# Kernel tuning notes

Measured on AMD Instinct MI355X. Metric: run time of the kernel, lower is better.

Reference implementation:

```python
import jax, jax.numpy as jnp
import numpy as np

CROP_H = 7
CROP_W = 7
EXTRAP = 0.0  # module hardcodes 0 when calling CropAndResizeFunction


def _crop_and_resize(image, boxes, box_ind):
    """TF-style crop_and_resize.
    image: (N,C,H,W) float; boxes: (M,4) normalized (y1,x1,y2,x2); box_ind: (M,) int32.
    Returns (M,C,CROP_H,CROP_W).
    """
    N, C, H, W = image.shape
    dt = image.dtype
    y1, x1, y2, x2 = boxes[:, 0], boxes[:, 1], boxes[:, 2], boxes[:, 3]
    ii = jnp.arange(CROP_H, dtype=dt)
    jj = jnp.arange(CROP_W, dtype=dt)
    # sample coordinates in feature-map space, shape (M, CROP_H) / (M, CROP_W)
    y = y1[:, None] * (H - 1) + ii[None, :] * ((y2 - y1) * (H - 1) / (CROP_H - 1))[:, None]
    x = x1[:, None] * (W - 1) + jj[None, :] * ((x2 - x1) * (W - 1) / (CROP_W - 1))[:, None]
    valid_y = (y >= 0) & (y <= H - 1)
    valid_x = (x >= 0) & (x <= W - 1)
    yt_f = jnp.floor(y)
    xt_f = jnp.floor(x)
    y_lerp = y - yt_f  # (M, oh)
    x_lerp = x - xt_f  # (M, ow)
    yt = jnp.clip(yt_f, 0, H - 1).astype(jnp.int32)
    yb = jnp.clip(jnp.ceil(y), 0, H - 1).astype(jnp.int32)
    xl = jnp.clip(xt_f, 0, W - 1).astype(jnp.int32)
    xr = jnp.clip(jnp.ceil(x), 0, W - 1).astype(jnp.int32)
    img = jnp.transpose(image, (0, 2, 3, 1))  # (N,H,W,C) for clean gather
    b = box_ind[:, None, None]                # (M,1,1)
    tl = img[b, yt[:, :, None], xl[:, None, :]]  # (M,oh,ow,C)
    tr = img[b, yt[:, :, None], xr[:, None, :]]
    bl = img[b, yb[:, :, None], xl[:, None, :]]
    br = img[b, yb[:, :, None], xr[:, None, :]]
    xl_w = x_lerp[:, None, :, None]
    top = tl + (tr - tl) * xl_w
    bot = bl + (br - bl) * xl_w
    out = top + (bot - top) * y_lerp[:, :, None, None]
    valid = (valid_y[:, :, None] & valid_x[:, None, :])[..., None]
    out = jnp.where(valid, out, jnp.asarray(EXTRAP, dt))
    return jnp.transpose(out, (0, 3, 1, 2))  # (M,C,oh,ow)


def setup_inputs() -> dict:
    key = jax.random.key(0)
    k0, k1, k2, k3, k4, k5 = jax.random.split(key, 6)
    N, C, H, W = 2, 256, 200, 304
    M = 2048
    scale = 0.0625  # 1/16
    Himg, Wimg = H / scale, W / scale
    featuremap = jax.random.normal(k0, (N, C, H, W), dtype=jnp.float32)
    x1 = jax.random.uniform(k1, (M, 1), minval=0.0, maxval=Wimg - 260.0)
    y1 = jax.random.uniform(k2, (M, 1), minval=0.0, maxval=Himg - 260.0)
    bw = jax.random.uniform(k3, (M, 1), minval=32.0, maxval=256.0)
    bh = jax.random.uniform(k4, (M, 1), minval=32.0, maxval=256.0)
    ids = jax.random.randint(k5, (M, 1), 0, N).astype(jnp.float32)
    rois = jnp.concatenate([ids, x1, y1, x1 + bw, y1 + bh], axis=1)
    return {"featuremap": featuremap, "rois": rois, "spatial_scale": jnp.float32(scale)}


def reference(featuremap, rois, spatial_scale):
    H, W = featuremap.shape[2], featuremap.shape[3]
    boxes = rois[:, 1:5] * spatial_scale
    box_ind = rois[:, 0].astype(jnp.int32)
    x1, y1, x2, y2 = boxes[:, 0], boxes[:, 1], boxes[:, 2], boxes[:, 3]
    spacing_w = (x2 - x1) / CROP_W
    spacing_h = (y2 - y1) / CROP_H
    nx0 = (x1 + spacing_w / 2 - 0.5) / (W - 1)
    ny0 = (y1 + spacing_h / 2 - 0.5) / (H - 1)
    nw = spacing_w * (CROP_W - 1) / (W - 1)
    nh = spacing_h * (CROP_H - 1) / (H - 1)
    boxes_n = jnp.stack([ny0, nx0, ny0 + nh, nx0 + nw], axis=1)
    return _crop_and_resize(featuremap, boxes_n, box_ind)
```

## Files before the change

### kernel.cpp

```cpp
#include <hip/hip_runtime.h>

#define RA_C   256
#define RA_H   200
#define RA_W   304
#define RA_HW  (RA_H * RA_W)
#define RA_CHW (RA_C * RA_HW)
#define CROPN  7
#define CROP2  (CROPN * CROPN)
#define OUT_M  (RA_C * CROP2)
#define BC     8
#define REG_R  16
#define REG_C  20
#define NF4    5
#define NTASK  (BC * REG_R * NF4)

__global__ __launch_bounds__(256) void roialign_kernel(
    const float* __restrict__ fm, const float* __restrict__ rois,
    const float* __restrict__ scale_p, float* __restrict__ out)
{
    __shared__ __align__(16) float s_reg[BC][REG_R][REG_C];
    __shared__ int   s_yt[CROPN], s_yb[CROPN], s_xl[CROPN], s_xr[CROPN];
    __shared__ float s_ylerp[CROPN], s_vy[CROPN], s_xlerp[CROPN], s_vx[CROPN];
    __shared__ int   s_imgbase;

    const int t = threadIdx.x;

    const int bid   = blockIdx.x;
    const int numBG = gridDim.x >> 5;
    const int xcd   = bid & 7;
    const int rb    = bid >> 3;
    const int cgl   = rb / numBG;
    const int m     = rb - cgl * numBG;
    const int c0    = (xcd * 4 + cgl) * BC;

    if (t < 2 * CROPN) {
        #pragma clang fp contract(off)
        {
            const int axis = (t >= CROPN) ? 1 : 0;
            const int k = axis ? (t - CROPN) : t;
            const float scale = scale_p[0];
            const float* rr = rois + (size_t)m * 5;
            if (t == 0) s_imgbase = (int)rr[0] * RA_CHW;
            float lo, hi, szm1;
            if (axis == 0) { lo = rr[2] * scale; hi = rr[4] * scale; szm1 = (float)(RA_H - 1); }
            else           { lo = rr[1] * scale; hi = rr[3] * scale; szm1 = (float)(RA_W - 1); }
            float sp   = (hi - lo) / 7.0f;
            float n0   = (lo + sp * 0.5f - 0.5f) / szm1;
            float nsz  = sp * 6.0f / szm1;
            float b2   = n0 + nsz;
            float d    = (b2 - n0) * szm1 / 6.0f;
            float coord = n0 * szm1 + (float)k * d;
            float fl = floorf(coord);
            float ce = ceilf(coord);
            float lerp = coord - fl;
            int lo_i = (int)fminf(fmaxf(fl, 0.0f), szm1);
            int hi_i = (int)fminf(fmaxf(ce, 0.0f), szm1);
            float valid = (coord >= 0.0f && coord <= szm1) ? 1.0f : 0.0f;
            if (axis == 0) {
                s_yt[k] = lo_i; s_yb[k] = hi_i;
                s_ylerp[k] = lerp; s_vy[k] = valid;
            } else {
                s_xl[k] = lo_i; s_xr[k] = hi_i;
                s_xlerp[k] = lerp; s_vx[k] = valid;
            }
        }
    }
    __syncthreads();

    const int ys   = s_yt[0];
    const int xs   = s_xl[0] & ~3;
    const int base = s_imgbase + c0 * RA_HW;

    #pragma unroll
    for (int s = 0; s < 3; ++s) {
        const int task = t + s * 256;
        if (task < NTASK) {
            const int cc  = task / (REG_R * NF4);
            const int rem = task - cc * (REG_R * NF4);
            const int rr2 = rem / NF4;
            const int kk  = rem - rr2 * NF4;
            const int row = min(ys + rr2, RA_H - 1);
            const int col = min(xs + 4 * kk, RA_W - 4);
            const float4 v = *reinterpret_cast<const float4*>(
                fm + (size_t)(base + cc * RA_HW + row * RA_W + col));
            *reinterpret_cast<float4*>(&s_reg[cc][rr2][4 * kk]) = v;
        }
    }
    __syncthreads();

    const int ij  = t & 63;
    const int ch2 = t >> 6;
    if (ij < CROP2) {
        const int i = ij / CROPN;
        const int j = ij - i * CROPN;
        const int rT = min(s_yt[i] - ys, REG_R - 1);
        const int rB = min(s_yb[i] - ys, REG_R - 1);
        const int cl = min(s_xl[j] - xs, REG_C - 1);
        const int cr = min(s_xr[j] - xs, REG_C - 1);
        const float yw = s_ylerp[i];
        const float xw = s_xlerp[j];
        const float vv = s_vy[i] * s_vx[j];
        float* __restrict__ op =
            out + (size_t)m * OUT_M + (size_t)(c0 + ch2 * 2) * CROP2 + ij;
        #pragma unroll
        for (int q = 0; q < 2; ++q) {
            const int cc = ch2 * 2 + q;
            const float tl = s_reg[cc][rT][cl];
            const float tr = s_reg[cc][rT][cr];
            const float bl = s_reg[cc][rB][cl];
            const float br = s_reg[cc][rB][cr];
            const float top = tl + (tr - tl) * xw;
            const float bot = bl + (br - bl) * xw;
            op[q * CROP2] = (top + (bot - top) * yw) * vv;
        }
    }
}

extern "C" void kernel_launch(void* const* d_in, const int* in_sizes, int n_in,
                              void* d_out, int out_size, void* d_ws, size_t ws_size,
                              hipStream_t stream) {
    const float* fm    = (const float*)d_in[0];
    const float* rois  = (const float*)d_in[1];
    const float* scale = (const float*)d_in[2];
    float* out = (float*)d_out;
    const int M = in_sizes[1] / 5;
    roialign_kernel<<<dim3(32 * M), dim3(256), 0, stream>>>(fm, rois, scale, out);
}
```

Before: 289.7 us.

## Process 16 channels per block, recompute tile origin, batch loads before shared stores

Each block now handles 16 channels instead of 8, which halves the grid to 16 blocks per ROI while keeping 256 threads. Every thread recomputes the region origin itself, so the first barrier before the global loads is gone and loads can start right away. Each 16-thread group issues five float4 loads into registers before writing them to padded shared memory. This should overlap memory latency better and cut block launch overhead, at the cost of more registers and fewer blocks in flight.

```diff
diff --git a/kernel.cpp b/kernel.cpp
--- a/kernel.cpp
+++ b/kernel.cpp
@@ -8,39 +8,38 @@
 #define CROPN  7
 #define CROP2  (CROPN * CROPN)
 #define OUT_M  (RA_C * CROP2)
-#define BC     8
+#define BC     16
 #define REG_R  16
 #define REG_C  20
 #define NF4    5
-#define NTASK  (BC * REG_R * NF4)
+#define CH_STR (REG_R * REG_C + 4)
 
 __global__ __launch_bounds__(256) void roialign_kernel(
     const float* __restrict__ fm, const float* __restrict__ rois,
     const float* __restrict__ scale_p, float* __restrict__ out)
 {
-    __shared__ __align__(16) float s_reg[BC][REG_R][REG_C];
+    __shared__ __align__(16) float s_reg[BC * CH_STR];
     __shared__ int   s_yt[CROPN], s_yb[CROPN], s_xl[CROPN], s_xr[CROPN];
     __shared__ float s_ylerp[CROPN], s_vy[CROPN], s_xlerp[CROPN], s_vx[CROPN];
-    __shared__ int   s_imgbase;
 
     const int t = threadIdx.x;
 
-    const int bid   = blockIdx.x;
-    const int numBG = gridDim.x >> 5;
-    const int xcd   = bid & 7;
-    const int rb    = bid >> 3;
-    const int cgl   = rb / numBG;
-    const int m     = rb - cgl * numBG;
-    const int c0    = (xcd * 4 + cgl) * BC;
+    const int bid  = blockIdx.x;
+    const int numB = gridDim.x >> 4;
+    const int xcd  = bid & 7;
+    const int rb   = bid >> 3;
+    const int cgl  = rb / numB;
+    const int m    = rb - cgl * numB;
+    const int c0   = (xcd * 2 + cgl) * BC;
+
+    const float scale = scale_p[0];
+    const float* __restrict__ rr = rois + (size_t)m * 5;
 
     if (t < 2 * CROPN) {
         #pragma clang fp contract(off)
         {
             const int axis = (t >= CROPN) ? 1 : 0;
             const int k = axis ? (t - CROPN) : t;
-            const float scale = scale_p[0];
-            const float* rr = rois + (size_t)m * 5;
-            if (t == 0) s_imgbase = (int)rr[0] * RA_CHW;
             float lo, hi, szm1;
             if (axis == 0) { lo = rr[2] * scale; hi = rr[4] * scale; szm1 = (float)(RA_H - 1); }
             else           { lo = rr[1] * scale; hi = rr[3] * scale; szm1 = (float)(RA_W - 1); }
@@ -65,31 +64,48 @@
             }
         }
     }
-    __syncthreads();
 
-    const int ys   = s_yt[0];
-    const int xs   = s_xl[0] & ~3;
-    const int base = s_imgbase + c0 * RA_HW;
+    int ys, xs, base;
+    {
+        #pragma clang fp contract(off)
+        float ylo = rr[2] * scale, yhi = rr[4] * scale;
+        float xlo = rr[1] * scale, xhi = rr[3] * scale;
+        float spy = (yhi - ylo) / 7.0f;
+        float n0y = (ylo + spy * 0.5f - 0.5f) / 199.0f;
+        float cy  = n0y * 199.0f;
+        float spx = (xhi - xlo) / 7.0f;
+        float n0x = (xlo + spx * 0.5f - 0.5f) / 303.0f;
+        float cx  = n0x * 303.0f;
+        ys = (int)fminf(fmaxf(floorf(cy), 0.0f), 199.0f);
+        xs = ((int)fminf(fmaxf(floorf(cx), 0.0f), 303.0f)) & ~3;
+        base = (int)rr[0] * RA_CHW + c0 * RA_HW;
+    }
 
+    const int cc  = t >> 4;
+    const int l16 = t & 15;
+    const float* __restrict__ cp = fm + (size_t)(base + cc * RA_HW);
+    float4 v[NF4];
     #pragma unroll
-    for (int s = 0; s < 3; ++s) {
-        const int task = t + s * 256;
-        if (task < NTASK) {
-            const int cc  = task / (REG_R * NF4);
-            const int rem = task - cc * (REG_R * NF4);
-            const int rr2 = rem / NF4;
-            const int kk  = rem - rr2 * NF4;
-            const int row = min(ys + rr2, RA_H - 1);
-            const int col = min(xs + 4 * kk, RA_W - 4);
-            const float4 v = *reinterpret_cast<const float4*>(
-                fm + (size_t)(base + cc * RA_HW + row * RA_W + col));
-            *reinterpret_cast<float4*>(&s_reg[cc][rr2][4 * kk]) = v;
+    for (int s = 0; s < NF4; ++s) {
+        const int idx = l16 + (s << 4);
+        const int r2  = idx / 5;
+        const int kk  = idx - r2 * 5;
+        const int row = min(ys + r2, RA_H - 1);
+        const int col = min(xs + (kk << 2), RA_W - 4);
+        v[s] = *reinterpret_cast<const float4*>(cp + row * RA_W + col);
+    }
+    {
+        float* __restrict__ sp_ = s_reg + cc * CH_STR;
+        #pragma unroll
+        for (int s = 0; s < NF4; ++s) {
+            const int idx = l16 + (s << 4);
+            *reinterpret_cast<float4*>(sp_ + (idx << 2)) = v[s];
         }
     }
     __syncthreads();
 
     const int ij  = t & 63;
-    const int ch2 = t >> 6;
+    const int ch4 = t >> 6;
     if (ij < CROP2) {
         const int i = ij / CROPN;
         const int j = ij - i * CROPN;
@@ -100,15 +116,17 @@
         const float yw = s_ylerp[i];
         const float xw = s_xlerp[j];
         const float vv = s_vy[i] * s_vx[j];
+        const int oT = rT * REG_C;
+        const int oB = rB * REG_C;
         float* __restrict__ op =
-            out + (size_t)m * OUT_M + (size_t)(c0 + ch2 * 2) * CROP2 + ij;
+            out + (size_t)m * OUT_M + (size_t)(c0 + ch4 * 4) * CROP2 + ij;
         #pragma unroll
-        for (int q = 0; q < 2; ++q) {
-            const int cc = ch2 * 2 + q;
-            const float tl = s_reg[cc][rT][cl];
-            const float tr = s_reg[cc][rT][cr];
-            const float bl = s_reg[cc][rB][cl];
-            const float br = s_reg[cc][rB][cr];
+        for (int q = 0; q < 4; ++q) {
+            const float* __restrict__ sp2 = s_reg + (ch4 * 4 + q) * CH_STR;
+            const float tl = sp2[oT + cl];
+            const float tr = sp2[oT + cr];
+            const float bl = sp2[oB + cl];
+            const float br = sp2[oB + cr];
             const float top = tl + (tr - tl) * xw;
             const float bot = bl + (br - bl) * xw;
             op[q * CROP2] = (top + (bot - top) * yw) * vv;
@@ -124,5 +142,5 @@
     const float* scale = (const float*)d_in[2];
     float* out = (float*)d_out;
     const int M = in_sizes[1] / 5;
-    roialign_kernel<<<dim3(32 * M), dim3(256), 0, stream>>>(fm, rois, scale, out);
+    roialign_kernel<<<dim3(16 * M), dim3(256), 0, stream>>>(fm, rois, scale, out);
 }
```

Measured after the change: 292.7 us. Within noise of the previous version (+1.1%).
